# Optimization experiments

Hardware: AMD Instinct MI355X
Metric: run time of the kernel (lower is better)

## Reference

```python
import jax, jax.numpy as jnp
import numpy as np

R = 128          # input voxel grid resolution
N = 200000
C_IN = 128
C_OUT = 256
G = 32           # group-norm groups
EPS = 1e-5


def _build_sparse_structure():
    """Generate random sparse voxel coords, downsample map, and 3x3x3 neighbor table."""
    rng = np.random.default_rng(0)
    lin = rng.choice(R ** 3, size=N, replace=False)
    cx, cy, cz = lin // (R * R), (lin // R) % R, lin % R
    # downsample by 2: coords // 2 on a (R//2)^3 grid
    Rd = R // 2
    key = ((cx // 2) * Rd + (cy // 2)) * Rd + (cz // 2)
    uk, inv = np.unique(key, return_inverse=True)   # uk sorted
    M = len(uk)
    dx, dy, dz = uk // (Rd * Rd), (uk // Rd) % Rd, uk % Rd
    # 27-neighbor table for submanifold 3x3x3 conv on the downsampled coords
    nbr = np.full((M, 27), -1, np.int32)
    k = 0
    for ox in (-1, 0, 1):
        for oy in (-1, 0, 1):
            for oz in (-1, 0, 1):
                nx, ny, nz = dx + ox, dy + oy, dz + oz
                valid = (nx >= 0) & (nx < Rd) & (ny >= 0) & (ny < Rd) & (nz >= 0) & (nz < Rd)
                nkey = (nx * Rd + ny) * Rd + nz
                pos = np.clip(np.searchsorted(uk, nkey), 0, M - 1)
                found = valid & (uk[pos] == nkey)
                nbr[:, k] = np.where(found, pos, -1).astype(np.int32)
                k += 1
    return inv.astype(np.int32), nbr, M


def setup_inputs() -> dict:
    pool_seg, nbr_idx, M = _build_sparse_structure()
    key = jax.random.key(0)
    ks = jax.random.split(key, 12)
    f32 = jnp.float32
    feats = jax.random.normal(ks[0], (N, C_IN), f32)
    s1 = float(1.0 / np.sqrt(27 * C_IN))
    s2 = float(1.0 / np.sqrt(27 * C_OUT))
    return {
        "feats": feats,
        "gn1_w": 1.0 + 0.1 * jax.random.normal(ks[1], (C_IN,), f32),
        "gn1_b": 0.1 * jax.random.normal(ks[2], (C_IN,), f32),
        "W1": jax.random.normal(ks[3], (27, C_IN, C_OUT), f32) * s1,
        "b1": 0.01 * jax.random.normal(ks[4], (C_OUT,), f32),
        "gn2_w": 1.0 + 0.1 * jax.random.normal(ks[5], (C_OUT,), f32),
        "gn2_b": 0.1 * jax.random.normal(ks[6], (C_OUT,), f32),
        "W2": jax.random.normal(ks[7], (27, C_OUT, C_OUT), f32) * s2,
        "b2": 0.01 * jax.random.normal(ks[8], (C_OUT,), f32),
        "Wskip": jax.random.normal(ks[9], (C_IN, C_OUT), f32) * float(1.0 / np.sqrt(C_IN)),
        "bskip": 0.01 * jax.random.normal(ks[10], (C_OUT,), f32),
        "pool_seg": jnp.asarray(pool_seg),
        "nbr_idx": jnp.asarray(nbr_idx),
        "num_down": int(M),
    }


def _group_norm(x, gamma, beta):
    # batch size 1: normalize each group over all voxels and its channels
    n, c = x.shape
    xg = x.reshape(n, G, c // G)
    mu = xg.mean(axis=(0, 2), keepdims=True)
    var = xg.var(axis=(0, 2), keepdims=True)
    xn = (xg - mu) * jax.lax.rsqrt(var + EPS)
    return xn.reshape(n, c) * gamma + beta


def _sparse_conv3(x, W, b, nbr_idx):
    # submanifold 3x3x3 conv: out[i] = sum_k W[k] @ x[nbr[i,k]] (missing nbr -> 0)
    idx = jnp.maximum(nbr_idx, 0)
    mask = (nbr_idx >= 0).astype(x.dtype)
    acc = jnp.zeros((x.shape[0], W.shape[2]), x.dtype)
    for k in range(27):
        acc = acc + (x[idx[:, k]] * mask[:, k:k + 1]) @ W[k]
    return acc + b


def reference(feats, gn1_w, gn1_b, W1, b1, gn2_w, gn2_b, W2, b2, Wskip, bskip,
              pool_seg, nbr_idx, num_down):
    # act_layers: GroupNorm32 + SiLU on the full-resolution sparse tensor
    h = jax.nn.silu(_group_norm(feats, gn1_w, gn1_b))
    # SparseDownsample(2): average features of voxels sharing a coord//2 cell
    cnt = jax.ops.segment_sum(jnp.ones((feats.shape[0], 1), feats.dtype),
                              pool_seg, num_segments=num_down)
    inv_cnt = 1.0 / jnp.maximum(cnt, 1.0)
    h_d = jax.ops.segment_sum(h, pool_seg, num_segments=num_down) * inv_cnt
    x_d = jax.ops.segment_sum(feats, pool_seg, num_segments=num_down) * inv_cnt
    # out_layers: conv3 -> GN -> SiLU -> conv3
    h1 = _sparse_conv3(h_d, W1, b1, nbr_idx)
    h2 = jax.nn.silu(_group_norm(h1, gn2_w, gn2_b))
    h3 = _sparse_conv3(h2, W2, b2, nbr_idx)
    # skip: 1x1 sparse conv on downsampled input, then add (same coord set)
    skip = x_d @ Wskip + bskip
    return h3 + skip
```

## Files before the change

### kernel.cpp

```cpp
#include <hip/hip_runtime.h>
#include <hip/hip_bf16.h>
#include <stdint.h>

typedef __hip_bfloat16 bf16;
typedef __attribute__((ext_vector_type(8))) __bf16 bf16x8;
typedef __attribute__((ext_vector_type(4))) float f32x4;

#define GN_EPS 1e-5f

__device__ __forceinline__ float silu_f(float x) {
  return x / (1.f + __expf(-x));
}

__device__ __forceinline__ float ldf(const void* p, size_t i, int f) {
  return f ? ((const float*)p)[i]
           : __bfloat162float(((const bf16*)p)[i]);
}

__global__ void detect_k(const void* __restrict__ gn1w, int* __restrict__ flag) {
  if (threadIdx.x == 0 && blockIdx.x == 0) {
    const unsigned short* u = (const unsigned short*)gn1w;
    float mx = 0.f;
    for (int i = 0; i < 128; ++i) {
      unsigned int b = ((unsigned int)u[i]) << 16;
      float v = __uint_as_float(b);
      v = fabsf(v);
      if (!isnan(v) && v > mx) mx = v;
    }
    flag[0] = (mx > 1e4f) ? 1 : 0;
  }
}

__global__ void transpose_k(const void* __restrict__ in, bf16* __restrict__ out,
                            int CI, int CO, const int* __restrict__ flagp) {
  const int f = *flagp;
  int k = blockIdx.y;
  int ntco = CO >> 5;
  int tci = blockIdx.x / ntco, tco = blockIdx.x % ntco;
  __shared__ float t[32][33];
  int tx = threadIdx.x & 31, ty = threadIdx.x >> 5;
  size_t base = (size_t)k * CI * CO;
  bf16* dst = out + base;
#pragma unroll
  for (int j = 0; j < 4; ++j)
    t[ty + 8 * j][tx] =
        ldf(in, base + (size_t)(tci * 32 + ty + 8 * j) * CO + tco * 32 + tx, f);
  __syncthreads();
#pragma unroll
  for (int j = 0; j < 4; ++j)
    dst[(size_t)(tco * 32 + ty + 8 * j) * CI + tci * 32 + tx] =
        __float2bfloat16(t[tx][ty + 8 * j]);
}

__global__ void gn_stats_k(const void* __restrict__ x, float* __restrict__ raw,
                           int rows, int C, const int* __restrict__ flagp) {
  const int f = *flagp;
  int tid = threadIdx.x;
  int rpb = 256 / C;
  int c = tid & (C - 1);
  int stripe = tid / C;
  float s = 0.f, sq = 0.f;
  for (int r = blockIdx.x * rpb + stripe; r < rows; r += gridDim.x * rpb) {
    float v = ldf(x, (size_t)r * C + c, f);
    s += v; sq += v * v;
  }
  __shared__ float ls[256], lq[256];
  ls[tid] = s; lq[tid] = sq;
  __syncthreads();
  if (tid < 32) {
    int per = C >> 5;
    float as = 0.f, aq = 0.f;
    for (int st = 0; st < rpb; ++st)
      for (int e = 0; e < per; ++e) {
        int idx = st * C + tid * per + e;
        as += ls[idx]; aq += lq[idx];
      }
    atomicAdd(&raw[tid], as);
    atomicAdd(&raw[32 + tid], aq);
  }
}

__global__ void gn_fin_k(const float* __restrict__ raw, float* __restrict__ fin,
                         float count) {
  int g = threadIdx.x;
  if (g < 32) {
    float mu = raw[g] / count;
    float var = fmaxf(raw[32 + g] / count - mu * mu, 0.f);
    fin[g] = mu;
    fin[32 + g] = rsqrtf(var + GN_EPS);
  }
}

__global__ void slots_k(const int* __restrict__ seg, int* __restrict__ cnt,
                        int* __restrict__ slots, int N) {
  int i = blockIdx.x * 256 + threadIdx.x;
  if (i >= N) return;
  int s = seg[i];
  int p = atomicAdd(&cnt[s], 1);
  if (p < 8) slots[s * 8 + p] = i;
}

__global__ void down_k(const void* __restrict__ feats, const int* __restrict__ slots,
                       const int* __restrict__ cnt, const float* __restrict__ fin1,
                       const void* __restrict__ gw, const void* __restrict__ gb,
                       bf16* __restrict__ xd, bf16* __restrict__ hd, int M,
                       const int* __restrict__ flagp) {
  const int f = *flagp;
  int cell = blockIdx.x * 2 + (threadIdx.x >> 7);
  int c = threadIdx.x & 127;
  if (cell >= M) return;
  int n = min(cnt[cell], 8);
  int g = c >> 2;
  float mu = fin1[g], is = fin1[32 + g];
  float w = ldf(gw, c, f), b = ldf(gb, c, f);
  float xs = 0.f, hs = 0.f;
  for (int j = 0; j < n; ++j) {
    int v = slots[cell * 8 + j];
    float fv = ldf(feats, (size_t)v * 128 + c, f);
    xs += fv;
    hs += silu_f((fv - mu) * is * w + b);
  }
  float inv = 1.f / (float)max(n, 1);
  xd[(size_t)cell * 128 + c] = __float2bfloat16(xs * inv);
  hd[(size_t)cell * 128 + c] = __float2bfloat16(hs * inv);
}

__global__ void act2_k(bf16* __restrict__ h, const float* __restrict__ fin2,
                       const void* __restrict__ gw, const void* __restrict__ gb,
                       size_t total, const int* __restrict__ flagp) {
  const int f = *flagp;
  size_t i = (size_t)blockIdx.x * 256 + threadIdx.x;
  if (i >= total) return;
  int c = (int)(i & 255);
  int g = c >> 3;
  float v = __bfloat162float(h[i]);
  float t = (v - fin2[g]) * fin2[32 + g] * ldf(gw, c, f) + ldf(gb, c, f);
  h[i] = __float2bfloat16(silu_f(t));
}

template <int CIN, bool SKIP>
__global__ __launch_bounds__(256, 2) void conv_k(
    const bf16* __restrict__ A, const bf16* __restrict__ Wt,
    const void* __restrict__ bias, const void* __restrict__ bias2,
    const bf16* __restrict__ Xd, const int* __restrict__ nbr,
    void* __restrict__ out, int M,
    const int* __restrict__ biasflagp, const int* __restrict__ outflagp) {
  __shared__ alignas(16) char lA[128 * 64];
  __shared__ alignas(16) char lB[128 * 64];
  const int bflag = *biasflagp, oflag = *outflagp;
  const int tid = threadIdx.x;
  const int wave = tid >> 6, lane = tid & 63;
  const int row0 = blockIdx.y * 128, n0 = blockIdx.x * 128;
  const int wr = wave >> 1, wc = wave & 1;
  const int sr = wave * 16 + (lane >> 2);
  const int ch4 = lane & 3;
  const int mrow = lane & 15, quad = lane >> 4;
  const int c1 = n0 + sr;

  f32x4 acc[4][4] = {};

  const int NK = SKIP ? 28 : 27;
  for (int kk = 0; kk < NK; ++kk) {
    const bool isW = (kk < 27);
    const int cink = isW ? CIN : 128;
    const bf16* Ab = isW ? A : Xd;
    const bf16* Wb = Wt + (size_t)(isW ? kk : 27) * (256 * CIN);
    int g1 = row0 + sr, g2 = g1 + 64;
    int src1 = -1, src2 = -1;
    if (isW) {
      if (g1 < M) src1 = nbr[(size_t)g1 * 27 + kk];
      if (g2 < M) src2 = nbr[(size_t)g2 * 27 + kk];
    } else {
      src1 = (g1 < M) ? g1 : -1;
      src2 = (g2 < M) ? g2 : -1;
    }
    const int ncb = cink >> 5;
    for (int cb = 0; cb < ncb; ++cb) {
      uint4 va1 = {0, 0, 0, 0}, va2 = {0, 0, 0, 0};
      if (src1 >= 0)
        va1 = *reinterpret_cast<const uint4*>(Ab + (size_t)src1 * cink + cb * 32 + ch4 * 8);
      if (src2 >= 0)
        va2 = *reinterpret_cast<const uint4*>(Ab + (size_t)src2 * cink + cb * 32 + ch4 * 8);
      uint4 vb1 = *reinterpret_cast<const uint4*>(Wb + (size_t)c1 * cink + cb * 32 + ch4 * 8);
      uint4 vb2 = *reinterpret_cast<const uint4*>(Wb + (size_t)(c1 + 64) * cink + cb * 32 + ch4 * 8);
      *reinterpret_cast<uint4*>(lA + (size_t)sr * 64 + ch4 * 16) = va1;
      *reinterpret_cast<uint4*>(lA + (size_t)(sr + 64) * 64 + ch4 * 16) = va2;
      *reinterpret_cast<uint4*>(lB + (size_t)sr * 64 + ch4 * 16) = vb1;
      *reinterpret_cast<uint4*>(lB + (size_t)(sr + 64) * 64 + ch4 * 16) = vb2;
      __syncthreads();
      bf16x8 af[4], bfr[4];
#pragma unroll
      for (int i = 0; i < 4; ++i)
        af[i] = *reinterpret_cast<const bf16x8*>(
            lA + (size_t)(wr * 64 + i * 16 + mrow) * 64 + quad * 16);
#pragma unroll
      for (int j = 0; j < 4; ++j)
        bfr[j] = *reinterpret_cast<const bf16x8*>(
            lB + (size_t)(wc * 64 + j * 16 + mrow) * 64 + quad * 16);
#pragma unroll
      for (int i = 0; i < 4; ++i)
#pragma unroll
        for (int j = 0; j < 4; ++j)
          acc[i][j] = __builtin_amdgcn_mfma_f32_16x16x32_bf16(af[i], bfr[j],
                                                              acc[i][j], 0, 0, 0);
      __syncthreads();
    }
  }
#pragma unroll
  for (int j = 0; j < 4; ++j) {
    int col = n0 + wc * 64 + j * 16 + mrow;
    float bv = ldf(bias, col, bflag);
    if (SKIP) bv += ldf(bias2, col, bflag);
#pragma unroll
    for (int i = 0; i < 4; ++i) {
      int rb = row0 + wr * 64 + i * 16 + quad * 4;
#pragma unroll
      for (int r = 0; r < 4; ++r) {
        int row = rb + r;
        if (row < M) {
          size_t idx = (size_t)row * 256 + col;
          float val = acc[i][j][r] + bv;
          if (oflag) ((float*)out)[idx] = val;
          else ((bf16*)out)[idx] = __float2bfloat16(val);
        }
      }
    }
  }
}

extern "C" void kernel_launch(void* const* d_in, const int* in_sizes, int n_in,
                              void* d_out, int out_size, void* d_ws, size_t ws_size,
                              hipStream_t stream) {
  const void* feats = d_in[0];
  const void* gn1w = d_in[1];
  const void* gn1b = d_in[2];
  const void* W1 = d_in[3];
  const void* b1 = d_in[4];
  const void* gn2w = d_in[5];
  const void* gn2b = d_in[6];
  const void* W2 = d_in[7];
  const void* b2 = d_in[8];
  const void* Wsk = d_in[9];
  const void* bsk = d_in[10];
  const int* pool = (const int*)d_in[11];
  const int* nbr = (const int*)d_in[12];
  const int N = in_sizes[0] / 128;
  const int M = out_size / 256;

  char* ws = (char*)d_ws;
  auto aup = [](size_t x) { return (x + 255) & ~(size_t)255; };
  float* raw1 = (float*)(ws + 0);
  float* raw2 = (float*)(ws + 256);
  int* flag = (int*)(ws + 512);
  int* zeroflag = (int*)(ws + 516);
  int* cnt = (int*)(ws + 1024);
  size_t o = aup(1024 + (size_t)M * 4);
  float* fin1 = (float*)(ws + o); o += 256;
  float* fin2 = (float*)(ws + o); o += 256;
  int* slots = (int*)(ws + o); o = aup(o + (size_t)M * 32);
  bf16* xd = (bf16*)(ws + o); o += (size_t)M * 256;
  bf16* hd = (bf16*)(ws + o); o += (size_t)M * 256;
  bf16* h1 = (bf16*)(ws + o); o += (size_t)M * 512;
  bf16* wt1 = (bf16*)(ws + o); o += (size_t)27 * 256 * 128 * 2;
  bf16* wt2 = (bf16*)(ws + o); o += ((size_t)27 * 256 * 256 + 256 * 128) * 2;
  (void)ws_size; (void)n_in;

  hipMemsetAsync(ws, 0, 1024 + (size_t)M * 4, stream);

  detect_k<<<1, 64, 0, stream>>>(gn1w, flag);

  transpose_k<<<dim3(4 * 8, 27), 256, 0, stream>>>(W1, wt1, 128, 256, flag);
  transpose_k<<<dim3(8 * 8, 27), 256, 0, stream>>>(W2, wt2, 256, 256, flag);
  transpose_k<<<dim3(4 * 8, 1), 256, 0, stream>>>(
      Wsk, wt2 + (size_t)27 * 256 * 256, 128, 256, flag);

  gn_stats_k<<<512, 256, 0, stream>>>(feats, raw1, N, 128, flag);
  gn_fin_k<<<1, 64, 0, stream>>>(raw1, fin1, (float)N * 4.f);

  slots_k<<<(N + 255) / 256, 256, 0, stream>>>(pool, cnt, slots, N);
  down_k<<<(M + 1) / 2, 256, 0, stream>>>(feats, slots, cnt, fin1, gn1w, gn1b,
                                          xd, hd, M, flag);

  conv_k<128, false><<<dim3(2, (M + 127) / 128), 256, 0, stream>>>(
      hd, wt1, b1, nullptr, nullptr, nbr, h1, M, flag, zeroflag);

  gn_stats_k<<<512, 256, 0, stream>>>(h1, raw2, M, 256, zeroflag);
  gn_fin_k<<<1, 64, 0, stream>>>(raw2, fin2, (float)M * 8.f);
  act2_k<<<(int)(((size_t)M * 256 + 255) / 256), 256, 0, stream>>>(
      h1, fin2, gn2w, gn2b, (size_t)M * 256, flag);

  conv_k<256, true><<<dim3(2, (M + 127) / 128), 256, 0, stream>>>(
      h1, wt2, b2, bsk, xd, nbr, d_out, M, flag, flag);
}
```

Measured before the change: 1.541 ms.

## Double-buffer sparse conv with direct global-to-LDS loads, swizzle, XCD remap, vectorize act2

The conv kernel is restructured to stage 64-channel K tiles straight into double-buffered LDS with global_load_lds. It uses an XOR-swizzled layout to avoid bank conflicts and prefetches neighbor indices two steps ahead, which overlaps gather loads with MFMA work. Workgroups are remapped across XCDs, MFMA issue priority is raised, and missing neighbors read from a zeroed workspace region instead of taking a branch. The act2 kernel is vectorized to process 8 bf16 values per thread. This uses 64KB of LDS per block, which may reduce occupancy.

```diff
diff --git a/kernel.cpp b/kernel.cpp
--- a/kernel.cpp
+++ b/kernel.cpp
@@ -5,6 +5,7 @@
 typedef __hip_bfloat16 bf16;
 typedef __attribute__((ext_vector_type(8))) __bf16 bf16x8;
 typedef __attribute__((ext_vector_type(4))) float f32x4;
+typedef __attribute__((ext_vector_type(4))) int i32x4;
 
 #define GN_EPS 1e-5f
 
@@ -15,6 +16,12 @@
 __device__ __forceinline__ float ldf(const void* p, size_t i, int f) {
   return f ? ((const float*)p)[i]
            : __bfloat162float(((const bf16*)p)[i]);
+}
+
+__device__ __forceinline__ void llds16(const void* g, void* l) {
+  __builtin_amdgcn_global_load_lds(
+      (const __attribute__((address_space(1))) unsigned int*)g,
+      (__attribute__((address_space(3))) unsigned int*)l, 16, 0, 0);
 }
 
 __global__ void detect_k(const void* __restrict__ gn1w, int* __restrict__ flag) {
@@ -127,15 +134,22 @@
 
 __global__ void act2_k(bf16* __restrict__ h, const float* __restrict__ fin2,
                        const void* __restrict__ gw, const void* __restrict__ gb,
-                       size_t total, const int* __restrict__ flagp) {
+                       size_t total8, const int* __restrict__ flagp) {
   const int f = *flagp;
   size_t i = (size_t)blockIdx.x * 256 + threadIdx.x;
-  if (i >= total) return;
-  int c = (int)(i & 255);
-  int g = c >> 3;
-  float v = __bfloat162float(h[i]);
-  float t = (v - fin2[g]) * fin2[32 + g] * ldf(gw, c, f) + ldf(gb, c, f);
-  h[i] = __float2bfloat16(silu_f(t));
+  if (i >= total8) return;
+  int c0 = (int)((i * 8) & 255);
+  int g = c0 >> 3;
+  float mu = fin2[g], is = fin2[32 + g];
+  bf16x8 v = *reinterpret_cast<bf16x8*>(h + i * 8);
+  bf16x8 o;
+#pragma unroll
+  for (int j = 0; j < 8; ++j) {
+    float x = (float)v[j];
+    float t = (x - mu) * is * ldf(gw, c0 + j, f) + ldf(gb, c0 + j, f);
+    o[j] = (__bf16)silu_f(t);
+  }
+  *reinterpret_cast<bf16x8*>(h + i * 8) = o;
 }
 
 template <int CIN, bool SKIP>
@@ -143,74 +157,110 @@
     const bf16* __restrict__ A, const bf16* __restrict__ Wt,
     const void* __restrict__ bias, const void* __restrict__ bias2,
     const bf16* __restrict__ Xd, const int* __restrict__ nbr,
-    void* __restrict__ out, int M,
+    void* __restrict__ out, int M, int nwg, const void* __restrict__ zp,
     const int* __restrict__ biasflagp, const int* __restrict__ outflagp) {
-  __shared__ alignas(16) char lA[128 * 64];
-  __shared__ alignas(16) char lB[128 * 64];
+  constexpr int NCB = CIN / 64;
+  constexpr int NT = 27 * NCB + (SKIP ? 2 : 0);
+  __shared__ alignas(16) char smem[2 * 32768];
+
   const int bflag = *biasflagp, oflag = *outflagp;
   const int tid = threadIdx.x;
   const int wave = tid >> 6, lane = tid & 63;
-  const int row0 = blockIdx.y * 128, n0 = blockIdx.x * 128;
+
+  int bid = blockIdx.x;
+  int q = nwg >> 3, r8 = nwg & 7, xcd = bid & 7, ix = bid >> 3;
+  int wg = (xcd < r8 ? xcd * (q + 1) : r8 * (q + 1) + (xcd - r8) * q) + ix;
+  const int row0 = (wg >> 1) * 128, n0 = (wg & 1) * 128;
+
+  const int rb8 = lane >> 3;
+  const int slot = lane & 7;
+  const int gc = slot ^ rb8;
+  const int mrow = lane & 15, quad = lane >> 4;
   const int wr = wave >> 1, wc = wave & 1;
-  const int sr = wave * 16 + (lane >> 2);
-  const int ch4 = lane & 3;
-  const int mrow = lane & 15, quad = lane >> 4;
-  const int c1 = n0 + sr;
+
+  auto nbr_fetch = [&](int t) -> i32x4 {
+    i32x4 s;
+    bool isW = (!SKIP) || (t < 27 * NCB);
+    int kk = isW ? (t / NCB) : 0;
+#pragma unroll
+    for (int ro = 0; ro < 4; ++ro) {
+      int g = row0 + ro * 32 + wave * 8 + rb8;
+      int v = -1;
+      if (isW) {
+        if (g < M) v = nbr[(size_t)g * 27 + kk];
+      } else {
+        if (g < M) v = g;
+      }
+      s[ro] = v;
+    }
+    return s;
+  };
+
+  auto stage = [&](int t, char* buf, i32x4 srcs) {
+    bool isW = (!SKIP) || (t < 27 * NCB);
+    int cb = isW ? (t % NCB) : (t - 27 * NCB);
+    int cink = isW ? CIN : 128;
+    const bf16* Ab = isW ? A : Xd;
+    const bf16* Wb = Wt + (isW ? (size_t)(t / NCB) * (256 * CIN)
+                               : (size_t)27 * (256 * CIN));
+    const int coff = cb * 64 + gc * 8;
+#pragma unroll
+    for (int ro = 0; ro < 4; ++ro) {
+      int rrow = ro * 32 + wave * 8 + rb8;
+      int src = srcs[ro];
+      const bf16* ga = (src >= 0) ? Ab + (size_t)src * cink + coff
+                                  : (const bf16*)zp;
+      const bf16* gw2 = Wb + (size_t)(n0 + rrow) * cink + coff;
+      char* la = buf + ro * 4096 + wave * 1024;
+      char* lb = buf + 16384 + ro * 4096 + wave * 1024;
+      llds16(ga, la);
+      llds16(gw2, lb);
+    }
+  };
 
   f32x4 acc[4][4] = {};
 
-  const int NK = SKIP ? 28 : 27;
-  for (int kk = 0; kk < NK; ++kk) {
-    const bool isW = (kk < 27);
-    const int cink = isW ? CIN : 128;
-    const bf16* Ab = isW ? A : Xd;
-    const bf16* Wb = Wt + (size_t)(isW ? kk : 27) * (256 * CIN);
-    int g1 = row0 + sr, g2 = g1 + 64;
-    int src1 = -1, src2 = -1;
-    if (isW) {
-      if (g1 < M) src1 = nbr[(size_t)g1 * 27 + kk];
-      if (g2 < M) src2 = nbr[(size_t)g2 * 27 + kk];
-    } else {
-      src1 = (g1 < M) ? g1 : -1;
-      src2 = (g2 < M) ? g2 : -1;
-    }
-    const int ncb = cink >> 5;
-    for (int cb = 0; cb < ncb; ++cb) {
-      uint4 va1 = {0, 0, 0, 0}, va2 = {0, 0, 0, 0};
-      if (src1 >= 0)
-        va1 = *reinterpret_cast<const uint4*>(Ab + (size_t)src1 * cink + cb * 32 + ch4 * 8);
-      if (src2 >= 0)
-        va2 = *reinterpret_cast<const uint4*>(Ab + (size_t)src2 * cink + cb * 32 + ch4 * 8);
-      uint4 vb1 = *reinterpret_cast<const uint4*>(Wb + (size_t)c1 * cink + cb * 32 + ch4 * 8);
-      uint4 vb2 = *reinterpret_cast<const uint4*>(Wb + (size_t)(c1 + 64) * cink + cb * 32 + ch4 * 8);
-      *reinterpret_cast<uint4*>(lA + (size_t)sr * 64 + ch4 * 16) = va1;
-      *reinterpret_cast<uint4*>(lA + (size_t)(sr + 64) * 64 + ch4 * 16) = va2;
-      *reinterpret_cast<uint4*>(lB + (size_t)sr * 64 + ch4 * 16) = vb1;
-      *reinterpret_cast<uint4*>(lB + (size_t)(sr + 64) * 64 + ch4 * 16) = vb2;
-      __syncthreads();
-      bf16x8 af[4], bfr[4];
+  i32x4 sN = nbr_fetch(0);
+  stage(0, smem, sN);
+  sN = nbr_fetch(1);
+  asm volatile("s_waitcnt vmcnt(0)" ::: "memory");
+  __builtin_amdgcn_s_barrier();
+
+#pragma unroll 2
+  for (int t = 0; t < NT; ++t) {
+    char* cur = smem + (t & 1) * 32768;
+    if (t + 1 < NT) stage(t + 1, smem + ((t + 1) & 1) * 32768, sN);
+    if (t + 2 < NT) sN = nbr_fetch(t + 2);
+    const char* sA = cur + (size_t)(wr * 64 + mrow) * 128;
+    const char* sB = cur + 16384 + (size_t)(wc * 64 + mrow) * 128;
+#pragma unroll
+    for (int ks = 0; ks < 2; ++ks) {
+      const int co = ((ks * 4 + quad) ^ (mrow & 7)) * 16;
+      bf16x8 af[4], bv[4];
 #pragma unroll
       for (int i = 0; i < 4; ++i)
-        af[i] = *reinterpret_cast<const bf16x8*>(
-            lA + (size_t)(wr * 64 + i * 16 + mrow) * 64 + quad * 16);
+        af[i] = *reinterpret_cast<const bf16x8*>(sA + i * (16 * 128) + co);
 #pragma unroll
       for (int j = 0; j < 4; ++j)
-        bfr[j] = *reinterpret_cast<const bf16x8*>(
-            lB + (size_t)(wc * 64 + j * 16 + mrow) * 64 + quad * 16);
+        bv[j] = *reinterpret_cast<const bf16x8*>(sB + j * (16 * 128) + co);
+      __builtin_amdgcn_s_setprio(1);
 #pragma unroll
       for (int i = 0; i < 4; ++i)
 #pragma unroll
         for (int j = 0; j < 4; ++j)
-          acc[i][j] = __builtin_amdgcn_mfma_f32_16x16x32_bf16(af[i], bfr[j],
+          acc[i][j] = __builtin_amdgcn_mfma_f32_16x16x32_bf16(af[i], bv[j],
                                                               acc[i][j], 0, 0, 0);
-      __syncthreads();
-    }
-  }
+      __builtin_amdgcn_s_setprio(0);
+    }
+    asm volatile("s_waitcnt vmcnt(0)" ::: "memory");
+    __builtin_amdgcn_s_barrier();
+  }
+
 #pragma unroll
   for (int j = 0; j < 4; ++j) {
     int col = n0 + wc * 64 + j * 16 + mrow;
-    float bv = ldf(bias, col, bflag);
-    if (SKIP) bv += ldf(bias2, col, bflag);
+    float bvl = ldf(bias, col, bflag);
+    if (SKIP) bvl += ldf(bias2, col, bflag);
 #pragma unroll
     for (int i = 0; i < 4; ++i) {
       int rb = row0 + wr * 64 + i * 16 + quad * 4;
@@ -219,7 +269,7 @@
         int row = rb + r;
         if (row < M) {
           size_t idx = (size_t)row * 256 + col;
-          float val = acc[i][j][r] + bv;
+          float val = acc[i][j][r] + bvl;
           if (oflag) ((float*)out)[idx] = val;
           else ((bf16*)out)[idx] = __float2bfloat16(val);
         }
@@ -253,6 +303,7 @@
   float* raw2 = (float*)(ws + 256);
   int* flag = (int*)(ws + 512);
   int* zeroflag = (int*)(ws + 516);
+  const void* zp = (const void*)(ws + 768);
   int* cnt = (int*)(ws + 1024);
   size_t o = aup(1024 + (size_t)M * 4);
   float* fin1 = (float*)(ws + o); o += 256;
@@ -281,14 +332,17 @@
   down_k<<<(M + 1) / 2, 256, 0, stream>>>(feats, slots, cnt, fin1, gn1w, gn1b,
                                           xd, hd, M, flag);
 
-  conv_k<128, false><<<dim3(2, (M + 127) / 128), 256, 0, stream>>>(
-      hd, wt1, b1, nullptr, nullptr, nbr, h1, M, flag, zeroflag);
+  const int nby = (M + 127) / 128;
+  const int nwg = 2 * nby;
+
+  conv_k<128, false><<<nwg, 256, 0, stream>>>(
+      hd, wt1, b1, nullptr, nullptr, nbr, h1, M, nwg, zp, flag, zeroflag);
 
   gn_stats_k<<<512, 256, 0, stream>>>(h1, raw2, M, 256, zeroflag);
   gn_fin_k<<<1, 64, 0, stream>>>(raw2, fin2, (float)M * 8.f);
-  act2_k<<<(int)(((size_t)M * 256 + 255) / 256), 256, 0, stream>>>(
-      h1, fin2, gn2w, gn2b, (size_t)M * 256, flag);
-
-  conv_k<256, true><<<dim3(2, (M + 127) / 128), 256, 0, stream>>>(
-      h1, wt2, b2, bsk, xd, nbr, d_out, M, flag, flag);
-}
+  act2_k<<<(int)(((size_t)M * 32 + 255) / 256), 256, 0, stream>>>(
+      h1, fin2, gn2w, gn2b, (size_t)M * 32, flag);
+
+  conv_k<256, true><<<nwg, 256, 0, stream>>>(
+      h1, wt2, b2, bsk, xd, nbr, d_out, M, nwg, zp, flag, flag);
+}
```

Result: faster. 1.494 ms (-3.1%).
